# Kernel tuning notes

Measured on AMD Instinct MI355X. Metric: run time of the kernel, lower is better.

The kernel has to match this reference:

```python
import jax, jax.numpy as jnp
import numpy as np

B, L, D = 4, 4096, 2048
DF = 4 * D
CAPACITY_RATIO = 0.5


def setup_inputs() -> dict:
    key = jax.random.key(0)
    ks = jax.random.split(key, 4)
    s = 0.02
    return {
        "x": jax.random.normal(ks[0], (B, L, D), dtype=jnp.float32),
        "w_r": jax.random.normal(ks[1], (D,), dtype=jnp.float32) * s,
        "b_r": jnp.zeros((), dtype=jnp.float32),
        "w1": jax.random.normal(ks[2], (D, DF), dtype=jnp.float32) * s,
        "b1": jnp.zeros((DF,), dtype=jnp.float32),
        "w2": jax.random.normal(ks[3], (DF, D), dtype=jnp.float32) * s,
        "b2": jnp.zeros((D,), dtype=jnp.float32),
    }


def reference(x, w_r, b_r, w1, b1, w2, b2):
    # MoD eval path: router scores -> top-k token indices -> gather ->
    # block (FFN) on selected tokens -> scatter back into zeros.
    b, l, d = x.shape
    k = int(l * CAPACITY_RATIO)
    scores = jnp.einsum("bld,d->bl", x, w_r) + b_r          # [B, L]
    _, idx = jax.lax.top_k(scores, k)                        # [B, k] int32
    x_sel = jnp.take_along_axis(x, idx[:, :, None], axis=1)  # [B, k, D]
    h = jax.nn.gelu(jnp.einsum("bkd,df->bkf", x_sel, w1) + b1)
    out_sel = jnp.einsum("bkf,fd->bkd", h, w2) + b2          # [B, k, D]
    batch_ix = jnp.arange(b)[:, None]                        # [B, 1]
    out = jnp.zeros_like(x).at[batch_ix, idx].set(out_sel)
    return out
```

## Files before the change

### kernel.cpp

```cpp
#include <hip/hip_runtime.h>

#define BB 4
#define LL 4096
#define DD 2048
#define DFF 8192
#define KSEL 2048
#define MROWS (BB * KSEL)

typedef __bf16 bf16x8 __attribute__((ext_vector_type(8)));
typedef float f32x4 __attribute__((ext_vector_type(4)));
typedef unsigned short u16x8 __attribute__((ext_vector_type(8)));

__device__ __forceinline__ unsigned short f2bf(float f) {
    union { float f; unsigned int u; } v; v.f = f;
    unsigned int u = v.u;
    unsigned int r = u + 0x7fffu + ((u >> 16) & 1u);
    return (unsigned short)(r >> 16);
}

__device__ __forceinline__ void gl2lds16(const void* g, void* l) {
    __builtin_amdgcn_global_load_lds(
        (const __attribute__((address_space(1))) void*)g,
        (__attribute__((address_space(3))) void*)l,
        16, 0, 0);
}

__global__ __launch_bounds__(256) void router_conv_kernel(
    const float* __restrict__ x, const float* __restrict__ wr,
    const float* __restrict__ br, float* __restrict__ scores,
    unsigned short* __restrict__ xbf)
{
    const int lane = threadIdx.x & 63;
    const int wave = threadIdx.x >> 6;
    const int tok = blockIdx.x * 4 + wave;
    const float* row = x + (long)tok * DD;
    unsigned short* orow = xbf + (long)tok * DD;
    double acc = 0.0;
#pragma unroll
    for (int it = 0; it < 4; ++it) {
        const int off = it * 512 + lane * 8;
        float4 xv = *(const float4*)(row + off);
        float4 xw = *(const float4*)(row + off + 4);
        float4 wv = *(const float4*)(wr + off);
        float4 ww = *(const float4*)(wr + off + 4);
        acc += (double)xv.x * wv.x + (double)xv.y * wv.y
             + (double)xv.z * wv.z + (double)xv.w * wv.w;
        acc += (double)xw.x * ww.x + (double)xw.y * ww.y
             + (double)xw.z * ww.z + (double)xw.w * ww.w;
        u16x8 o;
        o[0] = f2bf(xv.x); o[1] = f2bf(xv.y); o[2] = f2bf(xv.z); o[3] = f2bf(xv.w);
        o[4] = f2bf(xw.x); o[5] = f2bf(xw.y); o[6] = f2bf(xw.z); o[7] = f2bf(xw.w);
        *(u16x8*)(orow + off) = o;
    }
#pragma unroll
    for (int o = 32; o > 0; o >>= 1) acc += __shfl_down(acc, o);
    if (lane == 0) scores[tok] = (float)(acc + (double)br[0]);
}

__global__ __launch_bounds__(256) void rank_select_kernel(
    const float* __restrict__ scores, int* __restrict__ idxout,
    int* __restrict__ zidxout)
{
    __shared__ float s[LL];
    const int b = blockIdx.y;
    const float* sb = scores + b * LL;
    for (int i = threadIdx.x; i < LL; i += 256) s[i] = sb[i];
    __syncthreads();
    const int t = blockIdx.x * 256 + threadIdx.x;
    const float my = s[t];
    int rank = 0;
#pragma unroll 16
    for (int j = 0; j < LL; ++j) {
        float sj = s[j];
        rank += (sj > my) || (sj == my && j < t);
    }
    if (rank < KSEL) idxout[(b << 11) + rank] = t;
    else             zidxout[(b << 11) + rank - KSEL] = t;
}

__global__ __launch_bounds__(256) void zero_rows_kernel(
    const int* __restrict__ zidx, float* __restrict__ Out)
{
    const int m = blockIdx.x;
    const int b = m >> 11;
    const int tok = zidx[m];
    float* dst = Out + ((long)b * LL + tok) * DD;
    const int c = threadIdx.x * 8;
    float4 z = {0.f, 0.f, 0.f, 0.f};
    *(float4*)(dst + c) = z;
    *(float4*)(dst + c + 4) = z;
}

__global__ __launch_bounds__(256) void conv_transpose2_kernel(
    const float* __restrict__ W1, unsigned short* __restrict__ W1t,
    const float* __restrict__ W2, unsigned short* __restrict__ W2t)
{
    __shared__ unsigned short t[64 * 72];
    int bid = blockIdx.x;
    const float* W; unsigned short* Wt; int KR, NC, bx, by;
    if (bid < 4096) { W = W1; Wt = W1t; KR = DD; NC = DFF; bx = bid & 127; by = bid >> 7; }
    else { bid -= 4096; W = W2; Wt = W2t; KR = DFF; NC = DD; bx = bid & 31; by = bid >> 5; }
    const int n0 = bx * 64;
    const int k0 = by * 64;
    const int tid = threadIdx.x;
    const int rk = tid >> 4;
    const int cn = (tid & 15) * 4;
#pragma unroll
    for (int p = 0; p < 4; ++p) {
        const int k = rk + p * 16;
        float4 v = *(const float4*)(W + (long)(k0 + k) * NC + n0 + cn);
        t[(cn + 0) * 72 + k] = f2bf(v.x);
        t[(cn + 1) * 72 + k] = f2bf(v.y);
        t[(cn + 2) * 72 + k] = f2bf(v.z);
        t[(cn + 3) * 72 + k] = f2bf(v.w);
    }
    __syncthreads();
    const int rn = tid >> 3;
    const int ck = (tid & 7) * 8;
#pragma unroll
    for (int p = 0; p < 2; ++p) {
        const int n = rn + p * 32;
        u16x8 o = *(const u16x8*)&t[n * 72 + ck];
        *(u16x8*)(Wt + (long)(n0 + n) * KR + k0 + ck) = o;
    }
}

template <int MODE, int IND>
__global__ __launch_bounds__(256, 4) void gemm_bt_kernel(
    const unsigned short* __restrict__ A,
    const unsigned short* __restrict__ Bt,
    const float* __restrict__ bias,
    unsigned short* __restrict__ H,
    const int* __restrict__ idx,
    float* __restrict__ Out,
    int K, int N)
{
    __shared__ unsigned short As[2 * 128 * 32];
    __shared__ unsigned short Bs[2 * 128 * 32];
    const int tid = threadIdx.x;
    const int lane = tid & 63;
    const int wave = tid >> 6;
    const int wm = wave >> 1, wn = wave & 1;

    const int npn = gridDim.x;
    const int pid = blockIdx.y * npn + blockIdx.x;
    const int per_grp = 32 * npn;
    const int gid = pid / per_grp;
    const int rem = pid - gid * per_grp;
    const int pm = gid * 32 + (rem & 31);
    const int pn = rem >> 5;
    const long m0 = (long)pm * 128;
    const long n0 = (long)pn * 128;

    const int c0 = wave * 128 + lane;
    const int c1 = c0 + 64;
    long ar0, ar1;
    if constexpr (IND) {
        const int r0 = (int)m0 + (c0 >> 2), r1 = (int)m0 + (c1 >> 2);
        ar0 = (long)(r0 >> 11) * LL + idx[r0];
        ar1 = (long)(r1 >> 11) * LL + idx[r1];
    } else {
        ar0 = m0 + (c0 >> 2);
        ar1 = m0 + (c1 >> 2);
    }
    const unsigned short* gA0 = A + ar0 * K + (c0 & 3) * 8;
    const unsigned short* gA1 = A + ar1 * K + (c1 & 3) * 8;
    const unsigned short* gB0 = Bt + (n0 + (c0 >> 2)) * K + (c0 & 3) * 8;
    const unsigned short* gB1 = Bt + (n0 + (c1 >> 2)) * K + (c1 & 3) * 8;
    unsigned short* lA0 = As + wave * 1024;
    unsigned short* lA1 = As + wave * 1024 + 512;
    unsigned short* lB0 = Bs + wave * 1024;
    unsigned short* lB1 = Bs + wave * 1024 + 512;

    f32x4 acc[4][4];
#pragma unroll
    for (int i = 0; i < 4; ++i)
#pragma unroll
        for (int j = 0; j < 4; ++j) {
            f32x4 z = {0.f, 0.f, 0.f, 0.f};
            acc[i][j] = z;
        }

    const int arow = wm * 64 + (lane & 15);
    const int brow = wn * 64 + (lane & 15);
    const int qk = (lane >> 4) * 8;

    for (int kt = 0; kt < K; kt += 64) {
#pragma unroll
        for (int h = 0; h < 2; ++h) {
            gl2lds16(gA0 + kt + 32 * h, lA0 + h * 4096);
            gl2lds16(gA1 + kt + 32 * h, lA1 + h * 4096);
            gl2lds16(gB0 + kt + 32 * h, lB0 + h * 4096);
            gl2lds16(gB1 + kt + 32 * h, lB1 + h * 4096);
        }
        __syncthreads();
#pragma unroll
        for (int s = 0; s < 2; ++s) {
            const unsigned short* as = As + s * 4096;
            const unsigned short* bs = Bs + s * 4096;
            bf16x8 af[4], bfm[4];
#pragma unroll
            for (int i = 0; i < 4; ++i)
                af[i] = *(const bf16x8*)&as[(arow + i * 16) * 32 + qk];
#pragma unroll
            for (int j = 0; j < 4; ++j)
                bfm[j] = *(const bf16x8*)&bs[(brow + j * 16) * 32 + qk];
#pragma unroll
            for (int i = 0; i < 4; ++i)
#pragma unroll
                for (int j = 0; j < 4; ++j)
                    acc[i][j] = __builtin_amdgcn_mfma_f32_16x16x32_bf16(
                        af[i], bfm[j], acc[i][j], 0, 0, 0);
        }
        __syncthreads();
    }

    const int colbase = (int)n0 + wn * 64 + (lane & 15);
    const long rowbase = m0 + wm * 64 + ((lane >> 4) << 2);

    if constexpr (MODE == 0) {
#pragma unroll
        for (int i = 0; i < 4; ++i) {
#pragma unroll
            for (int j = 0; j < 4; ++j) {
                const int col = colbase + j * 16;
                const float bv = bias[col];
#pragma unroll
                for (int r = 0; r < 4; ++r) {
                    const long row = rowbase + i * 16 + r;
                    float v = acc[i][j][r] + bv;
                    float u = v + 0.044715f * v * v * v;
                    float e = __expf(1.5957691216057308f * u);
                    float g = v - v * __builtin_amdgcn_rcpf(1.0f + e);
                    H[row * N + col] = f2bf(g);
                }
            }
        }
    } else {
        long obase[4][4];
#pragma unroll
        for (int i = 0; i < 4; ++i)
#pragma unroll
            for (int r = 0; r < 4; ++r) {
                const int row = (int)(rowbase + i * 16 + r);
                const int b = row >> 11;
                const int rr = row & (KSEL - 1);
                const int tok = idx[(b << 11) + rr];
                obase[i][r] = ((long)(b * LL + tok)) * DD;
            }
#pragma unroll
        for (int j = 0; j < 4; ++j) {
            const int col = colbase + j * 16;
            const float bv = bias[col];
#pragma unroll
            for (int i = 0; i < 4; ++i)
#pragma unroll
                for (int r = 0; r < 4; ++r)
                    Out[obase[i][r] + col] = acc[i][j][r] + bv;
        }
    }
}

extern "C" void kernel_launch(void* const* d_in, const int* in_sizes, int n_in,
                              void* d_out, int out_size, void* d_ws, size_t ws_size,
                              hipStream_t stream)
{
    const float* x  = (const float*)d_in[0];
    const float* wr = (const float*)d_in[1];
    const float* br = (const float*)d_in[2];
    const float* w1 = (const float*)d_in[3];
    const float* b1 = (const float*)d_in[4];
    const float* w2 = (const float*)d_in[5];
    const float* b2 = (const float*)d_in[6];
    float* out = (float*)d_out;

    char* ws = (char*)d_ws;
    float* scores = (float*)ws;              ws += (long)BB * LL * 4;
    int* idx  = (int*)ws;                    ws += (long)BB * KSEL * 4;
    int* zidx = (int*)ws;                    ws += (long)BB * (LL - KSEL) * 4;
    unsigned short* xbf  = (unsigned short*)ws; ws += (long)BB * LL * DD * 2;
    unsigned short* w1t  = (unsigned short*)ws; ws += (long)DFF * DD * 2;
    unsigned short* w2t  = (unsigned short*)ws; ws += (long)DD * DFF * 2;
    unsigned short* h    = (unsigned short*)ws; ws += (long)MROWS * DFF * 2;

    router_conv_kernel<<<(BB * LL) / 4, 256, 0, stream>>>(x, wr, br, scores, xbf);
    conv_transpose2_kernel<<<8192, 256, 0, stream>>>(w1, w1t, w2, w2t);
    rank_select_kernel<<<dim3(LL / 256, BB), 256, 0, stream>>>(scores, idx, zidx);
    zero_rows_kernel<<<BB * (LL - KSEL), 256, 0, stream>>>(zidx, out);
    gemm_bt_kernel<0, 1><<<dim3(DFF / 128, MROWS / 128), 256, 0, stream>>>(
        xbf, w1t, b1, h, idx, nullptr, DD, DFF);
    gemm_bt_kernel<1, 0><<<dim3(DD / 128, MROWS / 128), 256, 0, stream>>>(
        h, w2t, b2, nullptr, idx, out, DFF, DD);
}
```

Baseline: 1.063 ms.

## Replace GEMM with 256x256-tile, 4-stage software-pipelined kernel with swizzled LDS

Rewrites the bf16 GEMM kernel to use 256x256 output tiles with 512 threads (8 waves, each computing 128x64), a 4-buffer LDS ring with asynchronous global-to-LDS loads issued several k-steps ahead, and explicit vmcnt waits and barriers instead of syncthreads. LDS addresses are XOR-swizzled to avoid bank conflicts, MFMA phases are raised in priority via s_setprio, and the workgroup-to-tile mapping is remapped across 8 groups for L2 locality. The aim is to hide global-load latency behind MFMA work and raise arithmetic intensity per tile. In exchange it uses far more LDS and registers per block, which lowers occupancy, and the hand-placed waitcnt counts are fragile.

```diff
diff --git a/kernel.cpp b/kernel.cpp
--- a/kernel.cpp
+++ b/kernel.cpp
@@ -125,8 +125,55 @@
     }
 }
 
+#define VM6 asm volatile("s_waitcnt vmcnt(6)" ::: "memory")
+#define VM4 asm volatile("s_waitcnt vmcnt(4)" ::: "memory")
+#define VM0 asm volatile("s_waitcnt vmcnt(0)" ::: "memory")
+#define NOSTG ((void)0)
+#define NOVM ((void)0)
+#define CFENCE asm volatile("" ::: "memory")
+
+#define STAGE_A(b, q, kt) gl2lds16(ga[q] + (kt), &As[b][(q) * 4096 + wave * 512])
+#define STAGE_B(b, q, kt) gl2lds16(gb[q] + (kt), &Bs[b][(q) * 4096 + wave * 512])
+
+#define PH0(curb, STG, VMW) do {                                              \
+    const char* ab_ = (const char*)&As[curb][0] + aoff;                       \
+    const char* bb_ = (const char*)&Bs[curb][0] + boff;                       \
+    bf16x8 af_[4];                                                            \
+    _Pragma("unroll") for (int i_ = 0; i_ < 4; ++i_)                          \
+        af_[i_] = *(const bf16x8*)(ab_ + i_ * 1024);                          \
+    _Pragma("unroll") for (int j_ = 0; j_ < 4; ++j_)                          \
+        bfr[j_] = *(const bf16x8*)(bb_ + j_ * 1024);                          \
+    STG;                                                                      \
+    VMW;                                                                      \
+    CFENCE; __builtin_amdgcn_s_barrier(); CFENCE;                             \
+    __builtin_amdgcn_s_setprio(1);                                            \
+    _Pragma("unroll") for (int i_ = 0; i_ < 4; ++i_)                          \
+        _Pragma("unroll") for (int j_ = 0; j_ < 4; ++j_)                      \
+            acc[i_][j_] = __builtin_amdgcn_mfma_f32_16x16x32_bf16(            \
+                af_[i_], bfr[j_], acc[i_][j_], 0, 0, 0);                      \
+    __builtin_amdgcn_s_setprio(0);                                            \
+    CFENCE; __builtin_amdgcn_s_barrier(); CFENCE;                             \
+} while (0)
+
+#define PH1(curb, STG, VMW) do {                                              \
+    const char* ab_ = (const char*)&As[curb][0] + aoff + 4096;                \
+    bf16x8 af_[4];                                                            \
+    _Pragma("unroll") for (int i_ = 0; i_ < 4; ++i_)                          \
+        af_[i_] = *(const bf16x8*)(ab_ + i_ * 1024);                          \
+    STG;                                                                      \
+    VMW;                                                                      \
+    CFENCE; __builtin_amdgcn_s_barrier(); CFENCE;                             \
+    __builtin_amdgcn_s_setprio(1);                                            \
+    _Pragma("unroll") for (int i_ = 0; i_ < 4; ++i_)                          \
+        _Pragma("unroll") for (int j_ = 0; j_ < 4; ++j_)                      \
+            acc[4 + i_][j_] = __builtin_amdgcn_mfma_f32_16x16x32_bf16(        \
+                af_[i_], bfr[j_], acc[4 + i_][j_], 0, 0, 0);                  \
+    __builtin_amdgcn_s_setprio(0);                                            \
+    CFENCE; __builtin_amdgcn_s_barrier(); CFENCE;                             \
+} while (0)
+
 template <int MODE, int IND>
-__global__ __launch_bounds__(256, 4) void gemm_bt_kernel(
+__global__ __launch_bounds__(512, 2) void gemm_pipe_kernel(
     const unsigned short* __restrict__ A,
     const unsigned short* __restrict__ Bt,
     const float* __restrict__ bias,
@@ -135,99 +182,105 @@
     float* __restrict__ Out,
     int K, int N)
 {
-    __shared__ unsigned short As[2 * 128 * 32];
-    __shared__ unsigned short Bs[2 * 128 * 32];
+    __shared__ unsigned short As[4][256 * 32];
+    __shared__ unsigned short Bs[4][256 * 32];
     const int tid = threadIdx.x;
     const int lane = tid & 63;
     const int wave = tid >> 6;
-    const int wm = wave >> 1, wn = wave & 1;
-
-    const int npn = gridDim.x;
-    const int pid = blockIdx.y * npn + blockIdx.x;
-    const int per_grp = 32 * npn;
-    const int gid = pid / per_grp;
-    const int rem = pid - gid * per_grp;
-    const int pm = gid * 32 + (rem & 31);
-    const int pn = rem >> 5;
-    const long m0 = (long)pm * 128;
-    const long n0 = (long)pn * 128;
-
-    const int c0 = wave * 128 + lane;
-    const int c1 = c0 + 64;
-    long ar0, ar1;
-    if constexpr (IND) {
-        const int r0 = (int)m0 + (c0 >> 2), r1 = (int)m0 + (c1 >> 2);
-        ar0 = (long)(r0 >> 11) * LL + idx[r0];
-        ar1 = (long)(r1 >> 11) * LL + idx[r1];
-    } else {
-        ar0 = m0 + (c0 >> 2);
-        ar1 = m0 + (c1 >> 2);
-    }
-    const unsigned short* gA0 = A + ar0 * K + (c0 & 3) * 8;
-    const unsigned short* gA1 = A + ar1 * K + (c1 & 3) * 8;
-    const unsigned short* gB0 = Bt + (n0 + (c0 >> 2)) * K + (c0 & 3) * 8;
-    const unsigned short* gB1 = Bt + (n0 + (c1 >> 2)) * K + (c1 & 3) * 8;
-    unsigned short* lA0 = As + wave * 1024;
-    unsigned short* lA1 = As + wave * 1024 + 512;
-    unsigned short* lB0 = Bs + wave * 1024;
-    unsigned short* lB1 = Bs + wave * 1024 + 512;
-
-    f32x4 acc[4][4];
-#pragma unroll
-    for (int i = 0; i < 4; ++i)
+    const int wm = wave >> 2;
+    const int wn = wave & 3;
+
+    const int NN = N >> 8;
+    const int nwg = (int)gridDim.x;
+    const int per = nwg >> 3;
+    const int wg = ((int)blockIdx.x & 7) * per + ((int)blockIdx.x >> 3);
+    const int gsz = 4 * NN;
+    const int gidx = wg / gsz;
+    const int rem = wg - gidx * gsz;
+    const int pm = gidx * 4 + (rem & 3);
+    const int pn = rem >> 2;
+    const long m0 = (long)pm * 256;
+    const long n0 = (long)pn * 256;
+
+    const int cr = tid >> 2;
+    const int cl = (tid & 3) ^ (cr & 3);
+    const unsigned short* ga[2];
+    const unsigned short* gb[2];
+#pragma unroll
+    for (int q = 0; q < 2; ++q) {
+        const int r = q * 128 + cr;
+        long ar;
+        if constexpr (IND) {
+            const int sel = (int)m0 + r;
+            ar = (long)(sel >> 11) * LL + idx[sel];
+        } else {
+            ar = m0 + r;
+        }
+        ga[q] = A + ar * (long)K + cl * 8;
+        gb[q] = Bt + (n0 + r) * (long)K + cl * 8;
+    }
+
+    const int l15 = lane & 15;
+    const int lg = lane >> 4;
+    const int ko = ((lg ^ (l15 & 3)) << 4);
+    const int aoff = (wm * 128 + l15) * 64 + ko;
+    const int boff = (wn * 64 + l15) * 64 + ko;
+
+    f32x4 acc[8][4];
+#pragma unroll
+    for (int i = 0; i < 8; ++i)
 #pragma unroll
         for (int j = 0; j < 4; ++j) {
             f32x4 z = {0.f, 0.f, 0.f, 0.f};
             acc[i][j] = z;
         }
-
-    const int arow = wm * 64 + (lane & 15);
-    const int brow = wn * 64 + (lane & 15);
-    const int qk = (lane >> 4) * 8;
-
-    for (int kt = 0; kt < K; kt += 64) {
-#pragma unroll
-        for (int h = 0; h < 2; ++h) {
-            gl2lds16(gA0 + kt + 32 * h, lA0 + h * 4096);
-            gl2lds16(gA1 + kt + 32 * h, lA1 + h * 4096);
-            gl2lds16(gB0 + kt + 32 * h, lB0 + h * 4096);
-            gl2lds16(gB1 + kt + 32 * h, lB1 + h * 4096);
-        }
-        __syncthreads();
-#pragma unroll
-        for (int s = 0; s < 2; ++s) {
-            const unsigned short* as = As + s * 4096;
-            const unsigned short* bs = Bs + s * 4096;
-            bf16x8 af[4], bfm[4];
-#pragma unroll
-            for (int i = 0; i < 4; ++i)
-                af[i] = *(const bf16x8*)&as[(arow + i * 16) * 32 + qk];
-#pragma unroll
-            for (int j = 0; j < 4; ++j)
-                bfm[j] = *(const bf16x8*)&bs[(brow + j * 16) * 32 + qk];
-#pragma unroll
-            for (int i = 0; i < 4; ++i)
-#pragma unroll
-                for (int j = 0; j < 4; ++j)
-                    acc[i][j] = __builtin_amdgcn_mfma_f32_16x16x32_bf16(
-                        af[i], bfm[j], acc[i][j], 0, 0, 0);
-        }
-        __syncthreads();
-    }
-
-    const int colbase = (int)n0 + wn * 64 + (lane & 15);
-    const long rowbase = m0 + wm * 64 + ((lane >> 4) << 2);
+    bf16x8 bfr[4];
+
+    const int NT = K >> 5;
+
+    STAGE_A(0, 0, 0);  STAGE_A(0, 1, 0);
+    STAGE_B(0, 0, 0);  STAGE_B(0, 1, 0);
+    STAGE_A(1, 0, 32); STAGE_A(1, 1, 32);
+    STAGE_B(1, 0, 32); STAGE_B(1, 1, 32);
+    STAGE_A(2, 0, 64); STAGE_A(2, 1, 64);
+    VM6;
+    CFENCE; __builtin_amdgcn_s_barrier(); CFENCE;
+
+    int kb = 64, ka = 96;
+    for (int t = 0; t < NT - 3; ++t) {
+        const int cur = t & 3, b2 = (t + 2) & 3, b3 = (t + 3) & 3;
+        PH0(cur, (STAGE_B(b2, 0, kb), STAGE_B(b2, 1, kb)), NOVM);
+        PH1(cur, (STAGE_A(b3, 0, ka), STAGE_A(b3, 1, ka)), VM6);
+        kb += 32; ka += 32;
+    }
+    {
+        const int cur = (NT - 3) & 3, b2 = (NT - 1) & 3;
+        PH0(cur, (STAGE_B(b2, 0, kb), STAGE_B(b2, 1, kb)), NOVM);
+        PH1(cur, NOSTG, VM4);
+    }
+    {
+        const int cur = (NT - 2) & 3;
+        PH0(cur, NOSTG, NOVM);
+        PH1(cur, NOSTG, VM0);
+    }
+    {
+        const int cur = (NT - 1) & 3;
+        PH0(cur, NOSTG, NOVM);
+        PH1(cur, NOSTG, NOVM);
+    }
 
     if constexpr (MODE == 0) {
-#pragma unroll
-        for (int i = 0; i < 4; ++i) {
+        const long rowb = m0 + wm * 128 + (lg << 2);
+        const int colb = (int)n0 + wn * 64 + l15;
+#pragma unroll
+        for (int i = 0; i < 8; ++i) {
 #pragma unroll
             for (int j = 0; j < 4; ++j) {
-                const int col = colbase + j * 16;
+                const int col = colb + j * 16;
                 const float bv = bias[col];
 #pragma unroll
                 for (int r = 0; r < 4; ++r) {
-                    const long row = rowbase + i * 16 + r;
+                    const long row = rowb + i * 16 + r;
                     float v = acc[i][j][r] + bv;
                     float u = v + 0.044715f * v * v * v;
                     float e = __expf(1.5957691216057308f * u);
@@ -237,26 +290,26 @@
             }
         }
     } else {
-        long obase[4][4];
-#pragma unroll
-        for (int i = 0; i < 4; ++i)
+        const int rowb = (int)m0 + wm * 128 + (lg << 2);
+        const int colb = (int)n0 + wn * 64 + l15;
+#pragma unroll
+        for (int i = 0; i < 8; ++i) {
+            int ob[4];
 #pragma unroll
             for (int r = 0; r < 4; ++r) {
-                const int row = (int)(rowbase + i * 16 + r);
+                const int row = rowb + i * 16 + r;
                 const int b = row >> 11;
-                const int rr = row & (KSEL - 1);
-                const int tok = idx[(b << 11) + rr];
-                obase[i][r] = ((long)(b * LL + tok)) * DD;
+                const int tok = idx[(b << 11) + (row & (KSEL - 1))];
+                ob[r] = (b * LL + tok) * DD;
             }
 #pragma unroll
-        for (int j = 0; j < 4; ++j) {
-            const int col = colbase + j * 16;
-            const float bv = bias[col];
-#pragma unroll
-            for (int i = 0; i < 4; ++i)
+            for (int j = 0; j < 4; ++j) {
+                const int col = colb + j * 16;
+                const float bv = bias[col];
 #pragma unroll
                 for (int r = 0; r < 4; ++r)
-                    Out[obase[i][r] + col] = acc[i][j][r] + bv;
+                    Out[(long)ob[r] + col] = acc[i][j][r] + bv;
+            }
         }
     }
 }
@@ -287,8 +340,8 @@
     conv_transpose2_kernel<<<8192, 256, 0, stream>>>(w1, w1t, w2, w2t);
     rank_select_kernel<<<dim3(LL / 256, BB), 256, 0, stream>>>(scores, idx, zidx);
     zero_rows_kernel<<<BB * (LL - KSEL), 256, 0, stream>>>(zidx, out);
-    gemm_bt_kernel<0, 1><<<dim3(DFF / 128, MROWS / 128), 256, 0, stream>>>(
+    gemm_pipe_kernel<0, 1><<<(MROWS / 256) * (DFF / 256), 512, 0, stream>>>(
         xbf, w1t, b1, h, idx, nullptr, DD, DFF);
-    gemm_bt_kernel<1, 0><<<dim3(DD / 128, MROWS / 128), 256, 0, stream>>>(
+    gemm_pipe_kernel<1, 0><<<(MROWS / 256) * (DD / 256), 512, 0, stream>>>(
         h, w2t, b2, nullptr, idx, out, DFF, DD);
 }
```

After: 955.0 us. 1.11x faster.
